# Optimization experiments

Hardware: AMD Instinct MI355X
Metric: run time of the kernel (lower is better)

The kernel has to match this reference:

```python
import jax, jax.numpy as jnp
import numpy as np
import math

B, S, D, H = 2, 2048, 1024, 16
HD = D // H  # head_dims = 64


def setup_inputs() -> dict:
    key = jax.random.key(0)
    ks = jax.random.split(key, 8)
    sc = 1.0 / math.sqrt(D)
    return {
        "queries": jax.random.normal(ks[0], (B, S, D), jnp.float32),
        "keys":    jax.random.normal(ks[1], (B, S, D), jnp.float32),
        "values":  jax.random.normal(ks[2], (B, S, D), jnp.float32),
        # causal mask: 1 where attending allowed, 0 where blocked (masked_fill on ==0)
        "mask": jnp.tril(jnp.ones((S, S), jnp.int32)),
        "Wq": jax.random.normal(ks[3], (D, D), jnp.float32) * sc,
        "bq": jnp.zeros((D,), jnp.float32),
        "Wk": jax.random.normal(ks[4], (D, D), jnp.float32) * sc,
        "bk": jnp.zeros((D,), jnp.float32),
        "Wv": jax.random.normal(ks[5], (D, D), jnp.float32) * sc,
        "bv": jnp.zeros((D,), jnp.float32),
        "Wo": jax.random.normal(ks[6], (D, D), jnp.float32) * sc,
        "bo": jnp.zeros((D,), jnp.float32),
    }


def _split_heads(x):
    # (B, S, D) -> (B, H, S, HD)
    return x.reshape(B, S, H, HD).transpose(0, 2, 1, 3)


def reference(queries, keys, values, mask, Wq, bq, Wk, bk, Wv, bv, Wo, bo):
    q = queries @ Wq + bq
    k = keys @ Wk + bk
    # NOTE: faithful to source quirk — V is projected from the ALREADY-PROJECTED keys
    # (original: keys = self.W_keys(keys); values = self.W_values(keys))
    v = k @ Wv + bv
    q, k, v = _split_heads(q), _split_heads(k), _split_heads(v)
    # naive full NxN attention, as in the source
    scores = jnp.einsum("bhqd,bhkd->bhqk", q, k) / math.sqrt(HD)
    scores = jnp.where(mask == 0, jnp.float32(-1e9), scores)
    probs = jax.nn.softmax(scores, axis=-1)
    attn = jnp.einsum("bhqk,bhkd->bhqd", probs, v)
    attn = attn.transpose(0, 2, 1, 3).reshape(B, S, D)
    return attn @ Wo + bo
```

## Files before the change

### kernel.cpp

```cpp
#include <hip/hip_runtime.h>

typedef unsigned short u16;
typedef unsigned int u32;
typedef __bf16 bf16x8 __attribute__((ext_vector_type(8)));
typedef float f32x4 __attribute__((ext_vector_type(4)));
typedef float f32x16 __attribute__((ext_vector_type(16)));
typedef unsigned int u32x4v __attribute__((ext_vector_type(4)));

#define MFMA16(a, b, c) __builtin_amdgcn_mfma_f32_16x16x32_bf16(a, b, c, 0, 0, 0)
#define MFMA32(a, b, c) __builtin_amdgcn_mfma_f32_32x32x16_bf16(a, b, c, 0, 0, 0)

__device__ __forceinline__ void gload16(const void* g, void* l) {
  __builtin_amdgcn_global_load_lds((const __attribute__((address_space(1))) void*)g,
                                   (__attribute__((address_space(3))) void*)l, 16, 0, 0);
}

__device__ __forceinline__ u16 f2bf(float f) {
  u32 u = __builtin_bit_cast(u32, f);
  u += 0x7fffu + ((u >> 16) & 1u);
  return (u16)(u >> 16);
}
__device__ __forceinline__ u32 pack2(float a, float b) {
  u32 r;
  asm("v_cvt_pk_bf16_f32 %0, %1, %2" : "=v"(r) : "v"(a), "v"(b));
  return r;
}

__global__ __launch_bounds__(256) void cvt_kernel(const float* __restrict__ q,
                                                  const float* __restrict__ k,
                                                  u16* __restrict__ qb,
                                                  u16* __restrict__ kb) {
  const float* src = blockIdx.y ? k : q;
  u16* dst = blockIdx.y ? kb : qb;
  size_t i = (size_t)blockIdx.x * 256 + threadIdx.x;
  float4 v = ((const float4*)src)[i];
  uint2 o;
  o.x = pack2(v.x, v.y);
  o.y = pack2(v.z, v.w);
  ((uint2*)dst)[i] = o;
}

__global__ __launch_bounds__(256) void wtrans_kernel(const float* W0, const float* W1,
                                                     const float* W2, const float* W3,
                                                     u16* T0, u16* T1, u16* T2, u16* T3) {
  int z = blockIdx.z;
  const float* W = z == 0 ? W0 : z == 1 ? W1 : z == 2 ? W2 : W3;
  u16* T = z == 0 ? T0 : z == 1 ? T1 : z == 2 ? T2 : T3;
  __shared__ float tile[64][65];
  int tr = blockIdx.y * 64, tc = blockIdx.x * 64;
  int tid = threadIdx.x;
  int c4 = (tid & 15) * 4, r0 = tid >> 4;
#pragma unroll
  for (int i = 0; i < 4; i++) {
    int r = r0 + i * 16;
    float4 v = *(const float4*)(W + (size_t)(tr + r) * 1024 + tc + c4);
    tile[r][c4 + 0] = v.x; tile[r][c4 + 1] = v.y;
    tile[r][c4 + 2] = v.z; tile[r][c4 + 3] = v.w;
  }
  __syncthreads();
#pragma unroll
  for (int i = 0; i < 2; i++) {
    int c = tid + i * 256;
    int n = c >> 3, kg = c & 7;
    uint4 o;
    o.x = pack2(tile[kg * 8 + 0][n], tile[kg * 8 + 1][n]);
    o.y = pack2(tile[kg * 8 + 2][n], tile[kg * 8 + 3][n]);
    o.z = pack2(tile[kg * 8 + 4][n], tile[kg * 8 + 5][n]);
    o.w = pack2(tile[kg * 8 + 6][n], tile[kg * 8 + 7][n]);
    *(uint4*)(T + (size_t)(tc + n) * 1024 + tr + kg * 8) = o;
  }
}

template <int MODE>
__global__ __launch_bounds__(256) void gemm_kernel(
    const u16* A0, const u16* B0, const float* bias0, void* C0, float scale0,
    const u16* A1, const u16* B1, const float* bias1, void* C1, float scale1,
    int M, int N, int K) {
  const u16* A = A0; const u16* Bt = B0; const float* bias = bias0; void* Cout = C0;
  float scale = scale0;
  if (blockIdx.z) { A = A1; Bt = B1; bias = bias1; Cout = C1; scale = scale1; }

  __shared__ __attribute__((aligned(16))) char sAB[49152];
  const int tid = threadIdx.x, lane = tid & 63, w = tid >> 6;
  const int l15 = lane & 15, quad = lane >> 4;
  const int wm = (w >> 1) * 64, wn = (w & 1) * 32;
  const int m0 = blockIdx.y * 128, n0 = blockIdx.x * 64;

  const int lrow = lane >> 3, lcg = (lane & 7) ^ lrow;
  const u16* aP[4]; const u16* bP[2];
#pragma unroll
  for (int i = 0; i < 4; i++)
    aP[i] = A + (size_t)(m0 + w * 32 + i * 8 + lrow) * K + lcg * 8;
#pragma unroll
  for (int i = 0; i < 2; i++)
    bP[i] = Bt + (size_t)(n0 + w * 16 + i * 8 + lrow) * K + lcg * 8;

  int aoff[4], boff[2];
#pragma unroll
  for (int t = 0; t < 4; t++) {
    int ra = wm + t * 16 + l15;
    aoff[t] = ra * 128 + ((quad ^ (ra & 7)) * 16);
  }
#pragma unroll
  for (int t = 0; t < 2; t++) {
    int rb = wn + t * 16 + l15;
    boff[t] = 16384 + rb * 128 + ((quad ^ (rb & 7)) * 16);
  }

#pragma unroll
  for (int i = 0; i < 4; i++) { gload16(aP[i], sAB + w * 4096 + i * 1024); aP[i] += 64; }
#pragma unroll
  for (int i = 0; i < 2; i++) { gload16(bP[i], sAB + 16384 + w * 2048 + i * 1024); bP[i] += 64; }

  f32x4 acc[4][2] = {};
  int cur = 0;
  for (int k = 0; k < K; k += 64) {
    __syncthreads();
    if (k + 64 < K) {
      char* dst = sAB + (cur ^ 1) * 24576;
#pragma unroll
      for (int i = 0; i < 4; i++) { gload16(aP[i], dst + w * 4096 + i * 1024); aP[i] += 64; }
#pragma unroll
      for (int i = 0; i < 2; i++) { gload16(bP[i], dst + 16384 + w * 2048 + i * 1024); bP[i] += 64; }
    }
    const char* buf = sAB + cur * 24576;
#pragma unroll
    for (int kt = 0; kt < 2; kt++) {
      bf16x8 af[4], bfr[2];
#pragma unroll
      for (int t = 0; t < 4; t++) af[t] = *(const bf16x8*)(buf + (aoff[t] ^ (kt * 64)));
#pragma unroll
      for (int t = 0; t < 2; t++) bfr[t] = *(const bf16x8*)(buf + (boff[t] ^ (kt * 64)));
#pragma unroll
      for (int mt = 0; mt < 4; mt++)
#pragma unroll
        for (int nt = 0; nt < 2; nt++)
          acc[mt][nt] = MFMA16(af[mt], bfr[nt], acc[mt][nt]);
    }
    cur ^= 1;
  }

#pragma unroll
  for (int nt = 0; nt < 2; nt++) {
    int col = n0 + wn + nt * 16 + l15;
    float bv = bias[col];
#pragma unroll
    for (int mt = 0; mt < 4; mt++) {
      int row = m0 + wm + mt * 16 + quad * 4;
      if (MODE == 0) {
        u16* C = (u16*)Cout;
#pragma unroll
        for (int r = 0; r < 4; r++)
          C[(size_t)(row + r) * N + col] = f2bf((acc[mt][nt][r] + bv) * scale);
      } else if (MODE == 1) {
        u16* C = (u16*)Cout;
        int hh = col >> 6, hd = col & 63;
        int bb = row >> 11, s = row & 2047;
        uint2 o;
        o.x = pack2((acc[mt][nt][0] + bv) * scale, (acc[mt][nt][1] + bv) * scale);
        o.y = pack2((acc[mt][nt][2] + bv) * scale, (acc[mt][nt][3] + bv) * scale);
        *(uint2*)(C + ((size_t)((bb * 16 + hh) * 64 + hd) * 2048 + s)) = o;
      } else {
        float* C = (float*)Cout;
#pragma unroll
        for (int r = 0; r < 4; r++)
          C[(size_t)(row + r) * N + col] = (acc[mt][nt][r] + bv) * scale;
      }
    }
  }
}

__global__ __launch_bounds__(256) void attn_kernel(const u16* __restrict__ qw,
                                                   const u16* __restrict__ kw,
                                                   const u16* __restrict__ vw,
                                                   u16* __restrict__ aout) {
  __shared__ __attribute__((aligned(16))) char sRed[32768];
  __shared__ float slq[4][64];
  const int bh = blockIdx.x, p = blockIdx.y;
  const int b = bh >> 4, h = bh & 15;
  const int tid = threadIdx.x, lane = tid & 63, w = tid >> 6;
  const int g = w & 1, kh = w >> 1;
  const int c = lane & 31, hi = lane >> 5;
  const u16* kb0 = kw + (size_t)(b * 2048) * 1024 + h * 64;
  const u16* vb0 = vw + (size_t)bh * 64 * 2048;

  const u16* kbase = kb0 + (size_t)(kh * 32 + c) * 1024 + hi * 8;
  const u16* vrow0 = vb0 + (size_t)(c) * 2048 + kh * 32 + hi * 8;
  const u16* vrow1 = vb0 + (size_t)(32 + c) * 2048 + kh * 32 + hi * 8;

  for (int phase = 0; phase < 2; ++phase) {
    const int t = phase ? (31 - p) : p;
    __syncthreads();

    bf16x8 qf[2][4];
#pragma unroll
    for (int qb2 = 0; qb2 < 2; qb2++) {
      const u16* qbase =
          qw + (size_t)(b * 2048 + t * 64 + qb2 * 32 + c) * 1024 + h * 64 + hi * 8;
#pragma unroll
      for (int kt = 0; kt < 4; kt++) qf[qb2][kt] = *(const bf16x8*)(qbase + kt * 16);
    }

    f32x16 o00 = {}, o01 = {}, o10 = {}, o11 = {};
    float ls0 = 0.f, ls1 = 0.f;

    bf16x8 kf[4], vf[2][2];
    auto loadKV = [&](int j) {
      const u16* kp = kbase + (size_t)j * 65536;
#pragma unroll
      for (int kt = 0; kt < 4; kt++) kf[kt] = *(const bf16x8*)(kp + kt * 16);
#pragma unroll
      for (int kt2 = 0; kt2 < 2; kt2++) {
        vf[0][kt2] = *(const bf16x8*)(vrow0 + j * 64 + kt2 * 16);
        vf[1][kt2] = *(const bf16x8*)(vrow1 + j * 64 + kt2 * 16);
      }
    };
    if (g <= t) loadKV(g);
    for (int j = g; j <= t; j += 2) {
      f32x16 S0 = {}, S1 = {};
      __builtin_amdgcn_s_setprio(1);
#pragma unroll
      for (int kt = 0; kt < 4; kt++) {
        S0 = MFMA32(kf[kt], qf[0][kt], S0);
        S1 = MFMA32(kf[kt], qf[1][kt], S1);
      }
      __builtin_amdgcn_s_setprio(0);
      const bool diag = (j == t);
      u32 pw0[8], pw1[8];
      auto epack = [&](const f32x16& S, int qc, u32* pw, float& ls) {
        float e[16];
#pragma unroll
        for (int rg = 0; rg < 16; rg++) {
          float ev = __builtin_amdgcn_exp2f(S[rg]);
          if (diag) {
            int row = kh * 32 + (rg & 3) + 8 * (rg >> 2) + 4 * hi;
            if (row > qc) ev = 0.f;
          }
          e[rg] = ev;
        }
        float sAcc = 0.f;
#pragma unroll
        for (int rg = 0; rg < 16; rg += 4)
          sAcc += (e[rg] + e[rg + 1]) + (e[rg + 2] + e[rg + 3]);
        ls += sAcc;
#pragma unroll
        for (int i = 0; i < 8; i++) pw[i] = pack2(e[2 * i], e[2 * i + 1]);
      };
      epack(S0, c, pw0, ls0);
      epack(S1, 32 + c, pw1, ls1);
      __builtin_amdgcn_s_setprio(1);
#pragma unroll
      for (int kt2 = 0; kt2 < 2; kt2++) {
        const int bb = kt2 * 4;
        auto a0 = __builtin_amdgcn_permlane32_swap(pw0[bb + 0], pw0[bb + 2], false, false);
        auto a1 = __builtin_amdgcn_permlane32_swap(pw0[bb + 1], pw0[bb + 3], false, false);
        u32x4v pq0 = {a0[0], a1[0], a0[1], a1[1]};
        bf16x8 pf0 = __builtin_bit_cast(bf16x8, pq0);
        auto b0 = __builtin_amdgcn_permlane32_swap(pw1[bb + 0], pw1[bb + 2], false, false);
        auto b1 = __builtin_amdgcn_permlane32_swap(pw1[bb + 1], pw1[bb + 3], false, false);
        u32x4v pq1 = {b0[0], b1[0], b0[1], b1[1]};
        bf16x8 pf1 = __builtin_bit_cast(bf16x8, pq1);
        o00 = MFMA32(vf[0][kt2], pf0, o00);
        o10 = MFMA32(vf[1][kt2], pf0, o10);
        o01 = MFMA32(vf[0][kt2], pf1, o01);
        o11 = MFMA32(vf[1][kt2], pf1, o11);
      }
      __builtin_amdgcn_s_setprio(0);
      if (j + 2 <= t) loadKV(j + 2);
    }

    ls0 += __shfl_xor(ls0, 32, 64);
    ls1 += __shfl_xor(ls1, 32, 64);
    slq[w][hi * 32 + c] = hi ? ls1 : ls0;
    {
      char* myr = sRed + w * 8192;
#pragma unroll
      for (int ch = 0; ch < 4; ch++) {
        f32x4 x0 = {o00[ch * 4 + 0], o00[ch * 4 + 1], o00[ch * 4 + 2], o00[ch * 4 + 3]};
        *(f32x4*)(myr + ch * 1024 + lane * 16) = x0;
        f32x4 x1 = {o01[ch * 4 + 0], o01[ch * 4 + 1], o01[ch * 4 + 2], o01[ch * 4 + 3]};
        *(f32x4*)(myr + 4096 + ch * 1024 + lane * 16) = x1;
      }
    }
    __syncthreads();
    const int qh = w & 1, cp = (w >> 1) * 2;
    const int q = qh * 32 + c;
    const float lt = (slq[0][q] + slq[1][q]) + (slq[2][q] + slq[3][q]);
    const float inv = 1.0f / lt;
    u16* outp = aout + (size_t)(b * 2048 + t * 64 + q) * 1024 + h * 64;
#pragma unroll
    for (int cc = 0; cc < 2; cc++) {
      const int ch = cp + cc;
      f32x4 s = {};
#pragma unroll
      for (int wv = 0; wv < 4; wv++) {
        f32x4 rr = *(const f32x4*)(sRed + wv * 8192 + qh * 4096 + ch * 1024 + lane * 16);
        s[0] += rr[0]; s[1] += rr[1]; s[2] += rr[2]; s[3] += rr[3];
      }
      uint2 ov;
      ov.x = pack2(s[0] * inv, s[1] * inv);
      ov.y = pack2(s[2] * inv, s[3] * inv);
      *(uint2*)(outp + ch * 8 + hi * 4) = ov;
    }
    __syncthreads();
    {
      char* myr = sRed + w * 8192;
#pragma unroll
      for (int ch = 0; ch < 4; ch++) {
        f32x4 x0 = {o10[ch * 4 + 0], o10[ch * 4 + 1], o10[ch * 4 + 2], o10[ch * 4 + 3]};
        *(f32x4*)(myr + ch * 1024 + lane * 16) = x0;
        f32x4 x1 = {o11[ch * 4 + 0], o11[ch * 4 + 1], o11[ch * 4 + 2], o11[ch * 4 + 3]};
        *(f32x4*)(myr + 4096 + ch * 1024 + lane * 16) = x1;
      }
    }
    __syncthreads();
#pragma unroll
    for (int cc = 0; cc < 2; cc++) {
      const int ch = cp + cc;
      f32x4 s = {};
#pragma unroll
      for (int wv = 0; wv < 4; wv++) {
        f32x4 rr = *(const f32x4*)(sRed + wv * 8192 + qh * 4096 + ch * 1024 + lane * 16);
        s[0] += rr[0]; s[1] += rr[1]; s[2] += rr[2]; s[3] += rr[3];
      }
      uint2 ov;
      ov.x = pack2(s[0] * inv, s[1] * inv);
      ov.y = pack2(s[2] * inv, s[3] * inv);
      *(uint2*)(outp + 32 + ch * 8 + hi * 4) = ov;
    }
  }
}

extern "C" void kernel_launch(void* const* d_in, const int* in_sizes, int n_in,
                              void* d_out, int out_size, void* d_ws, size_t ws_size,
                              hipStream_t stream) {
  const float* queries = (const float*)d_in[0];
  const float* keys    = (const float*)d_in[1];
  const float* Wq = (const float*)d_in[4];
  const float* bq = (const float*)d_in[5];
  const float* Wk = (const float*)d_in[6];
  const float* bk = (const float*)d_in[7];
  const float* Wv = (const float*)d_in[8];
  const float* bv = (const float*)d_in[9];
  const float* Wo = (const float*)d_in[10];
  const float* bo = (const float*)d_in[11];

  char* ws = (char*)d_ws;
  u16* qb  = (u16*)(ws);
  u16* kb  = (u16*)(ws + (8u << 20));
  u16* qP  = (u16*)(ws + (16u << 20));
  u16* kP  = (u16*)(ws);
  u16* vP  = (u16*)(ws + (8u << 20));
  u16* WqT = (u16*)(ws + (24u << 20));
  u16* WkT = (u16*)(ws + (26u << 20));
  u16* WvT = (u16*)(ws + (28u << 20));
  u16* WoT = (u16*)(ws + (30u << 20));

  const float kscale = 1.4426950408889634f / 8.0f;

  cvt_kernel<<<dim3(4096, 2), 256, 0, stream>>>(queries, keys, qb, kb);
  wtrans_kernel<<<dim3(16, 16, 4), 256, 0, stream>>>(Wq, Wk, Wv, Wo, WqT, WkT, WvT, WoT);
  gemm_kernel<0><<<dim3(16, 32, 2), 256, 0, stream>>>(
      qb, WqT, bq, qP, kscale, kb, WkT, bk, kP, 1.0f, 4096, 1024, 1024);
  gemm_kernel<1><<<dim3(16, 32, 1), 256, 0, stream>>>(
      kP, WvT, bv, vP, 1.0f, kP, WvT, bv, vP, 1.0f, 4096, 1024, 1024);
  attn_kernel<<<dim3(32, 16), 256, 0, stream>>>(qP, kP, vP, qP);
  gemm_kernel<2><<<dim3(16, 32, 1), 256, 0, stream>>>(
      qP, WoT, bo, d_out, 1.0f, qP, WoT, bo, d_out, 1.0f, 4096, 1024, 1024);
}
```

Baseline: 228.1 us.

## Stage K tiles into swizzled LDS ring via async global-to-LDS loads

```diff
diff --git a/kernel.cpp b/kernel.cpp
--- a/kernel.cpp
+++ b/kernel.cpp
@@ -170,23 +170,40 @@
   }
 }
 
-__global__ __launch_bounds__(256) void attn_kernel(const u16* __restrict__ qw,
-                                                   const u16* __restrict__ kw,
-                                                   const u16* __restrict__ vw,
-                                                   u16* __restrict__ aout) {
-  __shared__ __attribute__((aligned(16))) char sRed[32768];
+__global__ __launch_bounds__(256, 2) void attn_kernel(const u16* __restrict__ qw,
+                                                      const u16* __restrict__ kw,
+                                                      const u16* __restrict__ vw,
+                                                      u16* __restrict__ aout) {
+  __shared__ __attribute__((aligned(16))) char sK[4][8192];
   __shared__ float slq[4][64];
+  char* sflat = (char*)sK;
   const int bh = blockIdx.x, p = blockIdx.y;
   const int b = bh >> 4, h = bh & 15;
   const int tid = threadIdx.x, lane = tid & 63, w = tid >> 6;
   const int g = w & 1, kh = w >> 1;
   const int c = lane & 31, hi = lane >> 5;
+  const int lrow = lane >> 3, lcg = (lane & 7) ^ lrow;
   const u16* kb0 = kw + (size_t)(b * 2048) * 1024 + h * 64;
   const u16* vb0 = vw + (size_t)bh * 64 * 2048;
 
-  const u16* kbase = kb0 + (size_t)(kh * 32 + c) * 1024 + hi * 8;
-  const u16* vrow0 = vb0 + (size_t)(c) * 2048 + kh * 32 + hi * 8;
+  int koffK[4];
+  {
+    int krow = kh * 32 + c;
+#pragma unroll
+    for (int kt = 0; kt < 4; kt++)
+      koffK[kt] = krow * 128 + (((kt * 2 + hi) ^ (krow & 7)) * 16);
+  }
+  const u16* vrow0 = vb0 + (size_t)c * 2048 + kh * 32 + hi * 8;
   const u16* vrow1 = vb0 + (size_t)(32 + c) * 2048 + kh * 32 + hi * 8;
+
+  auto stage = [&](int j, int slot) {
+    char* dst = sK[slot];
+#pragma unroll
+    for (int i = 0; i < 2; i++) {
+      int rr = w * 16 + i * 8 + lrow;
+      gload16(kb0 + (size_t)(j * 64 + rr) * 1024 + lcg * 8, dst + w * 2048 + i * 1024);
+    }
+  };
 
   for (int phase = 0; phase < 2; ++phase) {
     const int t = phase ? (31 - p) : p;
@@ -200,80 +217,87 @@
 #pragma unroll
       for (int kt = 0; kt < 4; kt++) qf[qb2][kt] = *(const bf16x8*)(qbase + kt * 16);
     }
+    stage(0, 0);
+    if (t >= 1) stage(1, 1);
 
     f32x16 o00 = {}, o01 = {}, o10 = {}, o11 = {};
     float ls0 = 0.f, ls1 = 0.f;
-
-    bf16x8 kf[4], vf[2][2];
-    auto loadKV = [&](int j) {
-      const u16* kp = kbase + (size_t)j * 65536;
-#pragma unroll
-      for (int kt = 0; kt < 4; kt++) kf[kt] = *(const bf16x8*)(kp + kt * 16);
-#pragma unroll
-      for (int kt2 = 0; kt2 < 2; kt2++) {
-        vf[0][kt2] = *(const bf16x8*)(vrow0 + j * 64 + kt2 * 16);
-        vf[1][kt2] = *(const bf16x8*)(vrow1 + j * 64 + kt2 * 16);
-      }
-    };
-    if (g <= t) loadKV(g);
-    for (int j = g; j <= t; j += 2) {
-      f32x16 S0 = {}, S1 = {};
-      __builtin_amdgcn_s_setprio(1);
-#pragma unroll
-      for (int kt = 0; kt < 4; kt++) {
-        S0 = MFMA32(kf[kt], qf[0][kt], S0);
-        S1 = MFMA32(kf[kt], qf[1][kt], S1);
-      }
-      __builtin_amdgcn_s_setprio(0);
-      const bool diag = (j == t);
-      u32 pw0[8], pw1[8];
-      auto epack = [&](const f32x16& S, int qc, u32* pw, float& ls) {
-        float e[16];
-#pragma unroll
-        for (int rg = 0; rg < 16; rg++) {
-          float ev = __builtin_amdgcn_exp2f(S[rg]);
-          if (diag) {
-            int row = kh * 32 + (rg & 3) + 8 * (rg >> 2) + 4 * hi;
-            if (row > qc) ev = 0.f;
+    const int R = (t + 2) >> 1;
+    for (int r = 0; r < R; ++r) {
+      __syncthreads();
+      const int jg = 2 * r + g;
+      bf16x8 vf00, vf01, vf10, vf11;
+      if (jg <= t) {
+        vf00 = *(const bf16x8*)(vrow0 + jg * 64);
+        vf01 = *(const bf16x8*)(vrow0 + jg * 64 + 16);
+        vf10 = *(const bf16x8*)(vrow1 + jg * 64);
+        vf11 = *(const bf16x8*)(vrow1 + jg * 64 + 16);
+      }
+      if (2 * r + 2 <= t) stage(2 * r + 2, (2 * r + 2) & 3);
+      if (2 * r + 3 <= t) stage(2 * r + 3, (2 * r + 3) & 3);
+      if (jg <= t) {
+        const char* buf = sK[jg & 3];
+        f32x16 S0 = {}, S1 = {};
+        __builtin_amdgcn_s_setprio(1);
+#pragma unroll
+        for (int kt = 0; kt < 4; kt++) {
+          bf16x8 kf = *(const bf16x8*)(buf + koffK[kt]);
+          S0 = MFMA32(kf, qf[0][kt], S0);
+          S1 = MFMA32(kf, qf[1][kt], S1);
+        }
+        __builtin_amdgcn_s_setprio(0);
+        const bool diag = (jg == t);
+        u32 pw0[8], pw1[8];
+        auto epack = [&](const f32x16& S, int qc, u32* pw, float& ls) {
+          float e[16];
+#pragma unroll
+          for (int rg = 0; rg < 16; rg++) {
+            float ev = __builtin_amdgcn_exp2f(S[rg]);
+            if (diag) {
+              int row = kh * 32 + (rg & 3) + 8 * (rg >> 2) + 4 * hi;
+              if (row > qc) ev = 0.f;
+            }
+            e[rg] = ev;
           }
-          e[rg] = ev;
+          float sAcc = 0.f;
+#pragma unroll
+          for (int rg = 0; rg < 16; rg += 4)
+            sAcc += (e[rg] + e[rg + 1]) + (e[rg + 2] + e[rg + 3]);
+          ls += sAcc;
+#pragma unroll
+          for (int i = 0; i < 8; i++) pw[i] = pack2(e[2 * i], e[2 * i + 1]);
+        };
+        epack(S0, c, pw0, ls0);
+        epack(S1, 32 + c, pw1, ls1);
+        __builtin_amdgcn_s_setprio(1);
+#pragma unroll
+        for (int kt2 = 0; kt2 < 2; kt2++) {
+          const int bb = kt2 * 4;
+          auto a0 = __builtin_amdgcn_permlane32_swap(pw0[bb + 0], pw0[bb + 2], false, false);
+          auto a1 = __builtin_amdgcn_permlane32_swap(pw0[bb + 1], pw0[bb + 3], false, false);
+          u32x4v pq0 = {a0[0], a1[0], a0[1], a1[1]};
+          bf16x8 pf0 = __builtin_bit_cast(bf16x8, pq0);
+          auto b0 = __builtin_amdgcn_permlane32_swap(pw1[bb + 0], pw1[bb + 2], false, false);
+          auto b1 = __builtin_amdgcn_permlane32_swap(pw1[bb + 1], pw1[bb + 3], false, false);
+          u32x4v pq1 = {b0[0], b1[0], b0[1], b1[1]};
+          bf16x8 pf1 = __builtin_bit_cast(bf16x8, pq1);
+          bf16x8 v0 = kt2 ? vf01 : vf00;
+          bf16x8 v1 = kt2 ? vf11 : vf10;
+          o00 = MFMA32(v0, pf0, o00);
+          o10 = MFMA32(v1, pf0, o10);
+          o01 = MFMA32(v0, pf1, o01);
+          o11 = MFMA32(v1, pf1, o11);
         }
-        float sAcc = 0.f;
-#pragma unroll
-        for (int rg = 0; rg < 16; rg += 4)
-          sAcc += (e[rg] + e[rg + 1]) + (e[rg + 2] + e[rg + 3]);
-        ls += sAcc;
-#pragma unroll
-        for (int i = 0; i < 8; i++) pw[i] = pack2(e[2 * i], e[2 * i + 1]);
-      };
-      epack(S0, c, pw0, ls0);
-      epack(S1, 32 + c, pw1, ls1);
-      __builtin_amdgcn_s_setprio(1);
-#pragma unroll
-      for (int kt2 = 0; kt2 < 2; kt2++) {
-        const int bb = kt2 * 4;
-        auto a0 = __builtin_amdgcn_permlane32_swap(pw0[bb + 0], pw0[bb + 2], false, false);
-        auto a1 = __builtin_amdgcn_permlane32_swap(pw0[bb + 1], pw0[bb + 3], false, false);
-        u32x4v pq0 = {a0[0], a1[0], a0[1], a1[1]};
-        bf16x8 pf0 = __builtin_bit_cast(bf16x8, pq0);
-        auto b0 = __builtin_amdgcn_permlane32_swap(pw1[bb + 0], pw1[bb + 2], false, false);
-        auto b1 = __builtin_amdgcn_permlane32_swap(pw1[bb + 1], pw1[bb + 3], false, false);
-        u32x4v pq1 = {b0[0], b1[0], b0[1], b1[1]};
-        bf16x8 pf1 = __builtin_bit_cast(bf16x8, pq1);
-        o00 = MFMA32(vf[0][kt2], pf0, o00);
-        o10 = MFMA32(vf[1][kt2], pf0, o10);
-        o01 = MFMA32(vf[0][kt2], pf1, o01);
-        o11 = MFMA32(vf[1][kt2], pf1, o11);
-      }
-      __builtin_amdgcn_s_setprio(0);
-      if (j + 2 <= t) loadKV(j + 2);
+        __builtin_amdgcn_s_setprio(0);
+      }
     }
 
     ls0 += __shfl_xor(ls0, 32, 64);
     ls1 += __shfl_xor(ls1, 32, 64);
+    __syncthreads();
     slq[w][hi * 32 + c] = hi ? ls1 : ls0;
     {
-      char* myr = sRed + w * 8192;
+      char* myr = sflat + w * 8192;
 #pragma unroll
       for (int ch = 0; ch < 4; ch++) {
         f32x4 x0 = {o00[ch * 4 + 0], o00[ch * 4 + 1], o00[ch * 4 + 2], o00[ch * 4 + 3]};
@@ -294,7 +318,7 @@
       f32x4 s = {};
 #pragma unroll
       for (int wv = 0; wv < 4; wv++) {
-        f32x4 rr = *(const f32x4*)(sRed + wv * 8192 + qh * 4096 + ch * 1024 + lane * 16);
+        f32x4 rr = *(const f32x4*)(sflat + wv * 8192 + qh * 4096 + ch * 1024 + lane * 16);
         s[0] += rr[0]; s[1] += rr[1]; s[2] += rr[2]; s[3] += rr[3];
       }
       uint2 ov;
@@ -304,7 +328,7 @@
     }
     __syncthreads();
     {
-      char* myr = sRed + w * 8192;
+      char* myr = sflat + w * 8192;
 #pragma unroll
       for (int ch = 0; ch < 4; ch++) {
         f32x4 x0 = {o10[ch * 4 + 0], o10[ch * 4 + 1], o10[ch * 4 + 2], o10[ch * 4 + 3]};
@@ -320,7 +344,7 @@
       f32x4 s = {};
 #pragma unroll
       for (int wv = 0; wv < 4; wv++) {
-        f32x4 rr = *(const f32x4*)(sRed + wv * 8192 + qh * 4096 + ch * 1024 + lane * 16);
+        f32x4 rr = *(const f32x4*)(sflat + wv * 8192 + qh * 4096 + ch * 1024 + lane * 16);
         s[0] += rr[0]; s[1] += rr[1]; s[2] += rr[2]; s[3] += rr[3];
       }
       uint2 ov;
```

Result: no change. 223.6 us (-2.0%).
